# Optimization experiments

Measured on AMD Instinct MI355X. Metric: run time of the kernel, lower is better.

Reference implementation:

```python
import jax, jax.numpy as jnp
import numpy as np

NUM_REQS = 4096      # active requests this step
K = 64               # new blocks appended per request
MAX_REQS = 8192      # rows in block table / num_blocks
MAX_BLOCKS = 4096    # columns per block-table row
G = 1                # num_kv_cache_groups
NUM_PHYS_BLOCKS = 1 << 20


def setup_inputs() -> dict:
    key = jax.random.key(0)
    k1, k2, k3, k4 = jax.random.split(key, 4)
    # unique request indices (kernel writes one row per batch element)
    req_indices = jax.random.permutation(k1, MAX_REQS)[:NUM_REQS].astype(jnp.int32)
    # cumulative new-block counts: exactly K per request
    cu_num_new_blocks = (jnp.arange(NUM_REQS + 1, dtype=jnp.int32) * K)[None, :]  # [G, num_reqs+1]
    new_block_ids = jax.random.randint(k2, (G, NUM_REQS * K), 0, NUM_PHYS_BLOCKS, dtype=jnp.int32)
    overwrite = jax.random.bernoulli(k3, 0.5, (NUM_REQS,))
    block_table_strides = jnp.full((G,), MAX_BLOCKS, dtype=jnp.int32)  # row stride per group
    block_table_ptrs = jnp.zeros((G,), dtype=jnp.int32)  # pointer indirection; modeled by block_tables directly
    # existing block counts, leave room for K appends
    num_blocks = jax.random.randint(k4, (G, MAX_REQS), 0, MAX_BLOCKS - K, dtype=jnp.int32)
    block_tables = jnp.zeros((MAX_REQS, MAX_BLOCKS), dtype=jnp.int32)
    return {
        "req_indices": req_indices,
        "cu_num_new_blocks": cu_num_new_blocks,
        "new_block_ids": new_block_ids,
        "overwrite": overwrite,
        "block_table_strides": block_table_strides,
        "block_table_ptrs": block_table_ptrs,
        "num_blocks": num_blocks,
        "block_tables": block_tables,
    }


def reference(req_indices, cu_num_new_blocks, new_block_ids, overwrite,
              block_table_strides, block_table_ptrs, num_blocks, block_tables):
    # Single KV-cache group (G=1): the group's base pointer/stride resolve to block_tables.
    cu = cu_num_new_blocks[0]                       # [num_reqs+1]
    counts = cu[1:] - cu[:-1]                       # [num_reqs] new blocks per batch element
    total = new_block_ids.shape[1]
    j = jnp.arange(total, dtype=jnp.int32)
    # batch element owning flat new-block slot j: largest b with cu[b] <= j
    b = (jnp.searchsorted(cu, j, side="right") - 1).astype(jnp.int32)
    # destination start per batch element: 0 on overwrite, else current length of the row
    dst_start = jnp.where(overwrite, 0, num_blocks[0, req_indices]).astype(jnp.int32)  # [num_reqs]
    rows = req_indices[b]                           # [total]
    cols = dst_start[b] + (j - cu[b])               # [total]
    block_tables_out = block_tables.at[rows, cols].set(new_block_ids[0])
    # num_blocks[g, req] = dst_start + num_new_blocks (kernel side effect)
    num_blocks_out = num_blocks.at[0, req_indices].set(dst_start + counts)
    return block_tables_out, num_blocks_out
```

## Files before the change

### kernel.cpp

```cpp
#include <hip/hip_runtime.h>

#define MAX_REQS   8192
#define MAX_BLOCKS 4096
#define NBT        (MAX_REQS * MAX_BLOCKS)

typedef int int4v __attribute__((ext_vector_type(4)));

__global__ void bt_copy_kernel(const int* __restrict__ bt_in,
                               const int* __restrict__ nb_in,
                               int* __restrict__ out) {
    const int4v* __restrict__ src = reinterpret_cast<const int4v*>(bt_in);
    int4v* __restrict__ dst = reinterpret_cast<int4v*>(out);
    const int n4 = NBT / 4;
    const int stride = gridDim.x * blockDim.x;
    int gid = blockIdx.x * blockDim.x + threadIdx.x;
    for (int i = gid; i < n4; i += stride) {
        dst[i] = src[i];
    }
    if (gid < MAX_REQS) {
        out[NBT + gid] = nb_in[gid];
    }
}

__global__ void bt_scatter_kernel(const int* __restrict__ req_indices,
                                  const int* __restrict__ cu,
                                  const int* __restrict__ new_ids,
                                  const int* __restrict__ overwrite,
                                  const int* __restrict__ strides,
                                  const int* __restrict__ nb_in,
                                  int* __restrict__ out,
                                  int num_reqs) {
    const int r = blockIdx.x;
    if (r >= num_reqs) return;
    const int start = cu[r];
    const int count = cu[r + 1] - start;
    const int row = req_indices[r];
    const int ow = overwrite[r];
    const int dst0 = ow ? 0 : nb_in[row];
    const long long base = (long long)row * (long long)strides[0];
    for (int j = threadIdx.x; j < count; j += blockDim.x) {
        out[base + dst0 + j] = new_ids[start + j];
    }
    if (threadIdx.x == 0) {
        out[NBT + row] = dst0 + count;
    }
}

extern "C" void kernel_launch(void* const* d_in, const int* in_sizes, int n_in,
                              void* d_out, int out_size, void* d_ws, size_t ws_size,
                              hipStream_t stream) {
    const int* req_indices = (const int*)d_in[0];
    const int* cu          = (const int*)d_in[1];
    const int* new_ids     = (const int*)d_in[2];
    const int* overwrite   = (const int*)d_in[3];
    const int* strides     = (const int*)d_in[4];
    const int* nb_in       = (const int*)d_in[6];
    const int* bt_in       = (const int*)d_in[7];
    int* out = (int*)d_out;

    const int num_reqs = in_sizes[0];

    bt_copy_kernel<<<2048, 256, 0, stream>>>(bt_in, nb_in, out);
    bt_scatter_kernel<<<num_reqs, 64, 0, stream>>>(req_indices, cu, new_ids, overwrite,
                                                   strides, nb_in, out, num_reqs);
}
```

Measured before the change: 45.86 us.

## Fuse block-table copy and scatter into one per-row kernel via inverse index

Replaces the separate full-table copy kernel and per-request scatter kernel with a single kernel that has one workgroup per table row. Each workgroup copies its row with nontemporal vector loads and stores, then looks up an inverse map from row to request and writes the new block ids into that row. The inverse map is built by a memset plus a small kernel in workspace. This removes the second pass over scattered rows and one dependent launch, at the cost of an extra memset and a tiny kernel launch, and it hardcodes the row stride instead of reading it from the strides input.

```diff
diff --git a/kernel.cpp b/kernel.cpp
--- a/kernel.cpp
+++ b/kernel.cpp
@@ -6,43 +6,44 @@
 
 typedef int int4v __attribute__((ext_vector_type(4)));
 
-__global__ void bt_copy_kernel(const int* __restrict__ bt_in,
-                               const int* __restrict__ nb_in,
-                               int* __restrict__ out) {
-    const int4v* __restrict__ src = reinterpret_cast<const int4v*>(bt_in);
-    int4v* __restrict__ dst = reinterpret_cast<int4v*>(out);
-    const int n4 = NBT / 4;
-    const int stride = gridDim.x * blockDim.x;
-    int gid = blockIdx.x * blockDim.x + threadIdx.x;
-    for (int i = gid; i < n4; i += stride) {
-        dst[i] = src[i];
-    }
-    if (gid < MAX_REQS) {
-        out[NBT + gid] = nb_in[gid];
-    }
+__global__ void build_inv_kernel(const int* __restrict__ req_indices,
+                                 int* __restrict__ inv, int num_reqs) {
+    int r = blockIdx.x * blockDim.x + threadIdx.x;
+    if (r < num_reqs) inv[req_indices[r]] = r;
 }
 
-__global__ void bt_scatter_kernel(const int* __restrict__ req_indices,
-                                  const int* __restrict__ cu,
-                                  const int* __restrict__ new_ids,
-                                  const int* __restrict__ overwrite,
-                                  const int* __restrict__ strides,
-                                  const int* __restrict__ nb_in,
-                                  int* __restrict__ out,
-                                  int num_reqs) {
-    const int r = blockIdx.x;
-    if (r >= num_reqs) return;
-    const int start = cu[r];
-    const int count = cu[r + 1] - start;
-    const int row = req_indices[r];
-    const int ow = overwrite[r];
-    const int dst0 = ow ? 0 : nb_in[row];
-    const long long base = (long long)row * (long long)strides[0];
-    for (int j = threadIdx.x; j < count; j += blockDim.x) {
-        out[base + dst0 + j] = new_ids[start + j];
+__global__ void __launch_bounds__(256)
+fused_row_kernel(const int* __restrict__ bt_in,
+                 const int* __restrict__ nb_in,
+                 const int* __restrict__ cu,
+                 const int* __restrict__ new_ids,
+                 const int* __restrict__ overwrite,
+                 const int* __restrict__ inv,
+                 int* __restrict__ out) {
+    const int row = blockIdx.x;
+    const long long rowbase = (long long)row * MAX_BLOCKS;
+    const int4v* __restrict__ src = reinterpret_cast<const int4v*>(bt_in + rowbase);
+    int4v* __restrict__ dst = reinterpret_cast<int4v*>(out + rowbase);
+
+    #pragma unroll
+    for (int i = 0; i < MAX_BLOCKS / 4 / 256; ++i) {
+        int idx = threadIdx.x + 256 * i;
+        int4v v = __builtin_nontemporal_load(&src[idx]);
+        __builtin_nontemporal_store(v, &dst[idx]);
     }
-    if (threadIdx.x == 0) {
-        out[NBT + row] = dst0 + count;
+
+    const int r = inv[row];
+    if (r >= 0) {
+        const int start = cu[r];
+        const int count = cu[r + 1] - start;
+        const int dst0 = overwrite[r] ? 0 : nb_in[row];
+        __syncthreads();
+        for (int j = threadIdx.x; j < count; j += 256) {
+            out[rowbase + dst0 + j] = new_ids[start + j];
+        }
+        if (threadIdx.x == 0) out[NBT + row] = dst0 + count;
+    } else {
+        if (threadIdx.x == 0) out[NBT + row] = nb_in[row];
     }
 }
 
@@ -53,14 +54,16 @@
     const int* cu          = (const int*)d_in[1];
     const int* new_ids     = (const int*)d_in[2];
     const int* overwrite   = (const int*)d_in[3];
-    const int* strides     = (const int*)d_in[4];
     const int* nb_in       = (const int*)d_in[6];
     const int* bt_in       = (const int*)d_in[7];
     int* out = (int*)d_out;
+    int* inv = (int*)d_ws;
 
     const int num_reqs = in_sizes[0];
 
-    bt_copy_kernel<<<2048, 256, 0, stream>>>(bt_in, nb_in, out);
-    bt_scatter_kernel<<<num_reqs, 64, 0, stream>>>(req_indices, cu, new_ids, overwrite,
-                                                   strides, nb_in, out, num_reqs);
+    hipMemsetAsync(inv, 0xFF, MAX_REQS * sizeof(int), stream);
+    build_inv_kernel<<<(num_reqs + 255) / 256, 256, 0, stream>>>(req_indices, inv, num_reqs);
+
+    fused_row_kernel<<<MAX_REQS, 256, 0, stream>>>(bt_in, nb_in, cu, new_ids,
+                                                   overwrite, inv, out);
 }
```

Result: slower. 54.10 us (+18.0%).
